# Performance work log

Measured on AMD Instinct MI355X. Metric: run time of the kernel, lower is better.

The kernel has to match this reference:

```python
import jax, jax.numpy as jnp
import numpy as np

EPS = 1e-12

def _l2norm(x):
    return x * jax.lax.rsqrt(jnp.maximum(jnp.sum(x * x, -1, keepdims=True), EPS))

def _reverse_seq(x, lens):
    # per-row reversal of the first `lens[b]` steps (tf.reverse_sequence semantics)
    T = x.shape[1]
    ar = jnp.arange(T)[None, :]
    idx = jnp.where(ar < lens[:, None], lens[:, None] - 1 - ar, ar)
    return jnp.take_along_axis(x, idx[:, :, None], axis=1)

def _lstm(x, lens, Wx, Wh, b):
    # x: [B,T,D]; outputs zeroed past lens, state frozen past lens (dynamic_rnn)
    B, T, _ = x.shape
    H = Wh.shape[0]
    xW = jnp.einsum('btd,dh->bth', x, Wx) + b  # [B,T,4H]
    def step(carry, inp):
        h, c = carry
        xw_t, t = inp
        gates = xw_t + h @ Wh
        i, f, g, o = jnp.split(gates, 4, axis=-1)
        c_new = jax.nn.sigmoid(f) * c + jax.nn.sigmoid(i) * jnp.tanh(g)
        h_new = jax.nn.sigmoid(o) * jnp.tanh(c_new)
        valid = (t < lens)[:, None]
        return (jnp.where(valid, h_new, h), jnp.where(valid, c_new, c)), jnp.where(valid, h_new, 0.0)
    z = jnp.zeros((B, H), x.dtype)
    _, outs = jax.lax.scan(step, (z, z), (xW.transpose(1, 0, 2), jnp.arange(T)))
    return outs.transpose(1, 0, 2)

def _bilstm(x, lens, Wx_f, Wh_f, b_f, Wx_b, Wh_b, b_b):
    fwd = _lstm(x, lens, Wx_f, Wh_f, b_f)
    bwd = _reverse_seq(_lstm(_reverse_seq(x, lens), lens, Wx_b, Wh_b, b_b), lens)
    return jnp.concatenate([fwd, bwd], -1)  # [B,T,2R]

def setup_inputs() -> dict:
    B, T, CTX, D, R, HA, TD = 4096, 80, 10, 300, 200, 100, 256
    V, NTOK, NTY, PL = 100000, 250, 113, 3
    ks = jax.random.split(jax.random.key(0), 16)
    f32 = jnp.float32
    return {
        'input_data': jax.random.randint(ks[0], (B, T), 0, V, jnp.int32),
        'entMentIndex': jax.random.randint(ks[1], (B, 5), 0, B * T, jnp.int32),
        'entCtxLeftIndex': jax.random.randint(ks[2], (B, CTX), 0, B * T, jnp.int32),
        'entCtxRightIndex': jax.random.randint(ks[3], (B, CTX), 0, B * T, jnp.int32),
        'entMentLent': jnp.full((B, 1), 5.0, f32),
        'ctxLeftLent': jnp.full((B, 1), float(CTX), f32),
        'ctxRightLent': jnp.full((B, 1), float(CTX), f32),
        'type_path': jax.random.randint(ks[4], (NTY, PL), 0, NTOK, jnp.int32),
        'word_embed': jax.random.normal(ks[5], (V, D), f32) * 0.1,
        'h_m': jax.random.normal(ks[6], (D, HA), f32) * 0.01,
        'h1': jax.random.normal(ks[7], (2 * R, HA), f32) * 0.01,
        'h2': jax.random.normal(ks[8], (HA, 1), f32) * 0.01,
        'Wx_f': jax.random.normal(ks[9], (D, 4 * R), f32) * 0.05,
        'Wh_f': jax.random.normal(ks[10], (R, 4 * R), f32) * 0.05,
        'b_f': jnp.zeros((4 * R,), f32),
        'Wx_b': jax.random.normal(ks[11], (D, 4 * R), f32) * 0.05,
        'Wh_b': jax.random.normal(ks[12], (R, 4 * R), f32) * 0.05,
        'b_b': jnp.zeros((4 * R,), f32),
        'dense_W': jax.random.normal(ks[13], (D + 2 * R, TD), f32) * 0.05,
        'dense_b': jnp.zeros((TD,), f32),
        'type_tok': jax.random.normal(ks[14], (NTOK, TD), f32) * 0.01,
    }

def reference(input_data, entMentIndex, entCtxLeftIndex, entCtxRightIndex,
              entMentLent, ctxLeftLent, ctxRightLent, type_path, word_embed,
              h_m, h1, h2, Wx_f, Wh_f, b_f, Wx_b, Wh_b, b_b,
              dense_W, dense_b, type_tok):
    D = word_embed.shape[1]
    # flattened sentence embeddings with zero padding row at the end
    flat = jnp.concatenate(
        [jnp.take(word_embed, input_data.reshape(-1), axis=0),
         jnp.zeros((1, D), word_embed.dtype)], 0)
    # mention feature: mean of mention word vectors
    f1 = jnp.take(flat, entMentIndex, axis=0).sum(1) / entMentLent  # [B,D]
    # context features via shared BiLSTM
    left = jnp.take(flat, entCtxLeftIndex, axis=0)
    right = jnp.take(flat, entCtxRightIndex, axis=0)
    f2 = _bilstm(left, ctxLeftLent[:, 0].astype(jnp.int32), Wx_f, Wh_f, b_f, Wx_b, Wh_b, b_b)
    f3 = _bilstm(right, ctxRightLent[:, 0].astype(jnp.int32), Wx_f, Wh_f, b_f, Wx_b, Wh_b, b_b)
    ctx = jnp.concatenate([f2, f3], 1)  # [B, 2*CTX, 2R]
    # attention pooling (non-BBN branch uses relu)
    att = jax.nn.relu(jnp.einsum('btr,rh->bth', ctx, h1) + (f1 @ h_m)[:, None, :])
    w = jax.nn.softmax((att @ h2)[:, :, 0], axis=-1)  # [B, 2*CTX]
    ctx_feat = jnp.einsum('btr,bt->br', ctx, w)
    feat = jnp.concatenate([f1, ctx_feat], 1)  # [B, D+2R]
    ent = _l2norm(jax.nn.relu(feat @ dense_W + dense_b))  # [B, TD]
    # type-path embeddings: sum token embeddings along path, l2-normalize
    type_pad = jnp.concatenate([type_tok, jnp.zeros((1, type_tok.shape[1]), type_tok.dtype)], 0)
    type_norm = _l2norm(jnp.take(type_pad, type_path, axis=0).sum(1))  # [NTY, TD]
    return ent @ type_norm.T  # [B, NTY]
```

## Files before the change

### kernel.cpp

```cpp
#include <hip/hip_runtime.h>
#include <hip/hip_bf16.h>

constexpr int B    = 4096;
constexpr int T    = 80;
constexpr int CTXN = 10;
constexpr int D    = 300;
constexpr int R    = 200;
constexpr int HA   = 100;
constexpr int TD   = 256;
constexpr int NTY  = 113;
constexpr int PL   = 3;
constexpr int NTOK = 250;
constexpr int CTX2 = 20;
constexpr int R2   = 400;
constexpr int FEAT = 700;

constexpr int XSB  = 320;
constexpr int KH   = 256;
constexpr int KW   = 576;
constexpr int NB   = 832;
constexpr int CTXS = 448;
constexpr int DREG = 224;
constexpr int F1S  = 320;
constexpr int FBS  = 704;
constexpr int FMS  = 128;
constexpr int MX   = 2 * B * CTXN;

typedef __attribute__((ext_vector_type(8))) short bf16x8;
typedef __attribute__((ext_vector_type(4))) float f32x4;

__device__ __forceinline__ ushort f2bf(float f) {
    union { float f; uint32_t u; } x{f};
    uint32_t r = x.u + 0x7fff + ((x.u >> 16) & 1);
    return (ushort)(r >> 16);
}
__device__ __forceinline__ float bf2f(ushort u) {
    union { uint32_t u; float f; } x{(uint32_t)u << 16};
    return x.f;
}
__device__ __forceinline__ float fsig(float x) {
    return __builtin_amdgcn_rcpf(1.f + __expf(-x));
}
__device__ __forceinline__ float ftanh(float x) {
    return 1.f - 2.f * __builtin_amdgcn_rcpf(__expf(2.f * x) + 1.f);
}

#define GLD_LDS(g, l) __builtin_amdgcn_global_load_lds( \
    (const __attribute__((address_space(1))) void*)(g), \
    (__attribute__((address_space(3))) void*)(l), 16, 0, 0)
#define GLD_LDS_NT(g, l) __builtin_amdgcn_global_load_lds( \
    (const __attribute__((address_space(1))) void*)(g), \
    (__attribute__((address_space(3))) void*)(l), 16, 0, 2)

constexpr int NWC = 2 * NB * KW;
__global__ void k_prepw3(const float* __restrict__ Wx_f, const float* __restrict__ Wh_f,
                         const float* __restrict__ bf_, const float* __restrict__ Wx_b,
                         const float* __restrict__ Wh_b, const float* __restrict__ bb_,
                         ushort* __restrict__ Wcat, float* __restrict__ biasb) {
    int gid = blockIdx.x * blockDim.x + threadIdx.x;
    if (gid < NWC) {
        int k = gid % KW;
        int q = gid / KW;
        int np = q % NB, dir = q / NB;
        int rb = np >> 6, g = (np >> 4) & 3, ri = np & 15;
        int r = rb * 16 + ri, col = g * 200 + r;
        float v = 0.f;
        if (r < R) {
            if (k < KH) {
                if (k < R) v = (dir ? Wh_b : Wh_f)[(size_t)k * 800 + col];
            } else {
                int kx = k - KH;
                if (kx < D) v = (dir ? Wx_b : Wx_f)[(size_t)kx * 800 + col];
            }
        }
        Wcat[gid] = f2bf(v);
    } else if (gid < NWC + 2 * NB) {
        int t = gid - NWC;
        int np = t % NB, dirb = t / NB;
        int rb = np >> 6, g = (np >> 4) & 3, ri = np & 15;
        int r = rb * 16 + ri, col = g * 200 + r;
        biasb[t] = (r < R) ? (dirb ? bb_ : bf_)[col] : 0.f;
    }
}

__global__ void k_preph1(const float* __restrict__ h1, ushort* __restrict__ h1t) {
    int gid = blockIdx.x * blockDim.x + threadIdx.x;
    if (gid >= FMS * CTXS) return;
    int k = gid % CTXS, n = gid / CTXS;
    float v = 0.f;
    if (n < HA) {
        if (k < DREG) {
            if (k < R) v = h1[(size_t)k * HA + n];
        } else {
            int r2 = k - DREG;
            if (r2 < R) v = h1[(size_t)(R + r2) * HA + n];
        }
    }
    h1t[gid] = f2bf(v);
}
__global__ void k_prephm(const float* __restrict__ h_m, ushort* __restrict__ h_mt) {
    int gid = blockIdx.x * blockDim.x + threadIdx.x;
    if (gid >= FMS * F1S) return;
    int k = gid % F1S, n = gid / F1S;
    float v = (n < HA && k < D) ? h_m[(size_t)k * HA + n] : 0.f;
    h_mt[gid] = f2bf(v);
}
__global__ void k_prepdw(const float* __restrict__ dW, ushort* __restrict__ dWt) {
    int gid = blockIdx.x * blockDim.x + threadIdx.x;
    if (gid >= TD * FBS) return;
    int k = gid % FBS, n = gid / FBS;
    float v = (k < FEAT) ? dW[(size_t)k * TD + n] : 0.f;
    dWt[gid] = f2bf(v);
}

__global__ void k_gatherb(const int* __restrict__ idxL, const int* __restrict__ idxR,
                          const int* __restrict__ input_data,
                          const float* __restrict__ we,
                          ushort* __restrict__ xb) {
    int row = blockIdx.x * 4 + (threadIdx.x >> 6);
    int lane = threadIdx.x & 63;
    if (row >= MX) return;
    int side = row / (B * CTXN);
    int bt = row % (B * CTXN);
    int idx = (side ? idxR : idxL)[bt];
    int w = (idx >= 0 && idx < B * T) ? input_data[idx] : -1;
    ushort* dst = xb + (size_t)row * XSB;
    if (lane < XSB / 8) {
        int e0 = lane * 8;
        ushort tmp[8];
        #pragma unroll
        for (int j = 0; j < 8; ++j) {
            int e = e0 + j;
            float f = (w >= 0 && e < D) ? we[(size_t)w * D + e] : 0.f;
            tmp[j] = f2bf(f);
        }
        *reinterpret_cast<bf16x8*>(dst + e0) = *reinterpret_cast<bf16x8*>(tmp);
    }
}

__global__ void k_f1(const int* __restrict__ ment_idx,
                     const float* __restrict__ ment_lent,
                     const int* __restrict__ input_data,
                     const float* __restrict__ we,
                     ushort* __restrict__ featb, ushort* __restrict__ f1b) {
    int b = blockIdx.x;
    __shared__ int wrow[5];
    if (threadIdx.x < 5) {
        int idx = ment_idx[b * 5 + threadIdx.x];
        wrow[threadIdx.x] = (idx >= 0 && idx < B * T) ? input_data[idx] : -1;
    }
    __syncthreads();
    float inv = 1.0f / ment_lent[b];
    for (int d = threadIdx.x; d < F1S; d += blockDim.x) {
        float s = 0.f;
        if (d < D) {
            #pragma unroll
            for (int j = 0; j < 5; ++j) {
                int w = wrow[j];
                if (w >= 0) s += we[(size_t)w * D + d];
            }
            s *= inv;
        }
        ushort u = f2bf(s);
        if (d < D) featb[(size_t)b * FBS + d] = u;
        f1b[(size_t)b * F1S + d] = u;
    }
}

template<int MODE>
__global__ __launch_bounds__(256) void k_mfma(
    const ushort* __restrict__ A, int lda,
    const ushort* __restrict__ Bt, int ldb,
    float* __restrict__ C, int ldc, int K,
    const float* __restrict__ aux) {
    __shared__ __align__(16) ushort As[128 * 64];
    __shared__ __align__(16) ushort Bs[64 * 64];
    int tid = threadIdx.x, wave = tid >> 6, lane = tid & 63;
    int m0 = blockIdx.y * 128, n0 = blockIdx.x * 64;
    int wr = wave >> 1, wc = wave & 1;
    f32x4 acc[4][2] = {};

    for (int k0 = 0; k0 < K; k0 += 64) {
        #pragma unroll
        for (int p = 0; p < 4; ++p) {
            int chunk = p * 4 + wave;
            int row = chunk * 8 + (lane >> 3);
            int ss = (lane & 7) ^ (row & 7);
            GLD_LDS(A + (size_t)(m0 + row) * lda + k0 + ss * 8, As + chunk * 512);
        }
        #pragma unroll
        for (int p = 0; p < 2; ++p) {
            int chunk = p * 4 + wave;
            int row = chunk * 8 + (lane >> 3);
            int ss = (lane & 7) ^ (row & 7);
            GLD_LDS(Bt + (size_t)(n0 + row) * ldb + k0 + ss * 8, Bs + chunk * 512);
        }
        __syncthreads();
        #pragma unroll
        for (int kk = 0; kk < 2; ++kk) {
            bf16x8 a[4], bf[2];
            #pragma unroll
            for (int m = 0; m < 4; ++m) {
                int r = wr * 64 + m * 16 + (lane & 15);
                int ss = (kk * 4 + (lane >> 4)) ^ (r & 7);
                a[m] = *(const bf16x8*)&As[r * 64 + ss * 8];
            }
            #pragma unroll
            for (int n = 0; n < 2; ++n) {
                int r = wc * 32 + n * 16 + (lane & 15);
                int ss = (kk * 4 + (lane >> 4)) ^ (r & 7);
                bf[n] = *(const bf16x8*)&Bs[r * 64 + ss * 8];
            }
            #pragma unroll
            for (int m = 0; m < 4; ++m)
                #pragma unroll
                for (int n = 0; n < 2; ++n)
                    acc[m][n] = __builtin_amdgcn_mfma_f32_16x16x32_bf16(a[m], bf[n], acc[m][n], 0, 0, 0);
        }
        __syncthreads();
    }
    #pragma unroll
    for (int m = 0; m < 4; ++m) {
        #pragma unroll
        for (int n = 0; n < 2; ++n) {
            int c = n0 + wc * 32 + n * 16 + (lane & 15);
            #pragma unroll
            for (int j = 0; j < 4; ++j) {
                int rr = m0 + wr * 64 + m * 16 + (lane >> 4) * 4 + j;
                float v = acc[m][n][j];
                if (MODE == 1) v = fmaxf(v + aux[c], 0.f);
                C[(size_t)rr * ldc + c] = v;
            }
        }
    }
}

__global__ __launch_bounds__(512, 1) void k_lstm(
    const ushort* __restrict__ xb,
    const ushort* __restrict__ Wcat,
    const float* __restrict__ biasb,
    const float* __restrict__ lentL, const float* __restrict__ lentR,
    ushort* __restrict__ ctxb) {
    __shared__ __align__(16) ushort hS[64 * 256];
    __shared__ __align__(16) ushort xS[64 * 320];
    __shared__ __align__(16) ushort wS[8][2][2048];
    __shared__ int lenS[64];
    __shared__ int xrowS[CTXN][64];

    const int tid = threadIdx.x, wave = tid >> 6, lane = tid & 63;
    const int bid = blockIdx.x, xcd = bid & 7;
    const int dir = xcd >> 2;
    const int idx = (xcd & 3) * 32 + (bid >> 3);
    const int side = idx >> 6, rg = idx & 63;
    const int b0 = rg * 64;
    const ushort* Wd = Wcat + (size_t)dir * NB * KW;
    const int rl = lane & 15, ch = lane >> 4;

    if (tid < 64) {
        int b = b0 + tid;
        int len = (int)((side ? lentR : lentL)[b]);
        len = min(max(len, 0), CTXN);
        lenS[tid] = len;
        for (int s = 0; s < CTXN; ++s) {
            int tt = dir ? ((s < len) ? (len - 1 - s) : s) : s;
            xrowS[s][tid] = (side * (B * CTXN) + b * CTXN + tt) * XSB;
        }
    }
    {
        uint4 zz{0, 0, 0, 0};
        for (int i = tid; i < 64 * 256 / 8; i += 512)
            reinterpret_cast<uint4*>(hS)[i] = zz;
    }

    const int nrb = (wave + 8 < 13) ? 2 : 1;
    float bias_[2][4];
    #pragma unroll
    for (int g = 0; g < 4; ++g) {
        bias_[0][g] = biasb[dir * NB + wave * 64 + g * 16 + rl];
        bias_[1][g] = (nrb > 1) ? biasb[dir * NB + (wave + 8) * 64 + g * 16 + rl] : 0.f;
    }
    float cst[2][16];
    #pragma unroll
    for (int i = 0; i < 2; ++i)
        #pragma unroll
        for (int j = 0; j < 16; ++j) cst[i][j] = 0.f;

    __syncthreads();

    #pragma unroll
    for (int i = 0; i < 5; ++i) {
        int chunk = wave * 5 + i;
        int p = chunk * 64 + lane;
        int row = p / 40, c8s = p - row * 40;
        int c8 = c8s ^ (row & 7);
        GLD_LDS_NT(xb + xrowS[0][row] + c8 * 8, xS + chunk * 512);
    }
    __syncthreads();

    float hnew[2][16];

    for (int s = 0; s < CTXN; ++s) {
        const int kstart = (s == 0) ? KH : 0;
        #pragma unroll
        for (int rbi = 0; rbi < 2; ++rbi) {
            if (rbi < nrb) {
                const int rb = rbi ? (wave + 8) : wave;
                const ushort* wb = Wd + (size_t)rb * 64 * KW;
                const int nit = (KW - kstart) >> 5;
                f32x4 acc[4][4];
                #pragma unroll
                for (int m = 0; m < 4; ++m)
                    #pragma unroll
                    for (int g = 0; g < 4; ++g) acc[m][g] = f32x4{0.f, 0.f, 0.f, 0.f};

                #pragma unroll
                for (int i = 0; i < 4; ++i) {
                    int p = i * 64 + lane;
                    int n = p >> 2, c8s = p & 3;
                    int c8 = c8s ^ ((n >> 1) & 3);
                    GLD_LDS(wb + (size_t)n * KW + kstart + c8 * 8, &wS[wave][0][0] + i * 512);
                }
                for (int t = 0; t < nit; ++t) {
                    int k0 = kstart + t * 32;
                    if (t + 1 < nit) {
                        int k1 = k0 + 32;
                        ushort* dst = &wS[wave][(t + 1) & 1][0];
                        #pragma unroll
                        for (int i = 0; i < 4; ++i) {
                            int p = i * 64 + lane;
                            int n = p >> 2, c8s = p & 3;
                            int c8 = c8s ^ ((n >> 1) & 3);
                            GLD_LDS(wb + (size_t)n * KW + k1 + c8 * 8, dst + i * 512);
                        }
                        asm volatile("s_waitcnt vmcnt(4)" ::: "memory");
                    } else {
                        asm volatile("s_waitcnt vmcnt(0)" ::: "memory");
                    }
                    const ushort* abase; int astr, kof;
                    if (k0 < KH) { abase = hS; astr = 256; kof = k0 >> 3; }
                    else         { abase = xS; astr = 320; kof = (k0 - KH) >> 3; }
                    bf16x8 af[4];
                    #pragma unroll
                    for (int m = 0; m < 4; ++m) {
                        int row = m * 16 + rl;
                        int g = (kof + ch) ^ (row & 7);
                        af[m] = *reinterpret_cast<const bf16x8*>(&abase[row * astr + g * 8]);
                    }
                    const ushort* wbuf = &wS[wave][t & 1][0];
                    bf16x8 bfr[4];
                    #pragma unroll
                    for (int g4 = 0; g4 < 4; ++g4) {
                        int col = g4 * 16 + rl;
                        int c8 = ch ^ ((rl >> 1) & 3);
                        bfr[g4] = *reinterpret_cast<const bf16x8*>(&wbuf[col * 32 + c8 * 8]);
                    }
                    #pragma unroll
                    for (int m = 0; m < 4; ++m)
                        #pragma unroll
                        for (int g4 = 0; g4 < 4; ++g4)
                            acc[m][g4] = __builtin_amdgcn_mfma_f32_16x16x32_bf16(
                                af[m], bfr[g4], acc[m][g4], 0, 0, 0);
                }
                #pragma unroll
                for (int m = 0; m < 4; ++m) {
                    #pragma unroll
                    for (int j = 0; j < 4; ++j) {
                        int row = m * 16 + ch * 4 + j;
                        float gi = acc[m][0][j] + bias_[rbi][0];
                        float gf = acc[m][1][j] + bias_[rbi][1];
                        float gg = acc[m][2][j] + bias_[rbi][2];
                        float go = acc[m][3][j] + bias_[rbi][3];
                        float si = fsig(gi), sf = fsig(gf), so = fsig(go);
                        float cn = sf * cst[rbi][m * 4 + j] + si * ftanh(gg);
                        float hn = so * ftanh(cn);
                        if (s < lenS[row]) cst[rbi][m * 4 + j] = cn;
                        hnew[rbi][m * 4 + j] = hn;
                    }
                }
            }
        }
        asm volatile("s_waitcnt lgkmcnt(0)" ::: "memory");
        __builtin_amdgcn_s_barrier();

        #pragma unroll
        for (int rbi = 0; rbi < 2; ++rbi) {
            if (rbi < nrb) {
                const int rb = wave + rbi * 8;
                const int r = rb * 16 + rl;
                #pragma unroll
                for (int m = 0; m < 4; ++m) {
                    #pragma unroll
                    for (int j = 0; j < 4; ++j) {
                        int row = m * 16 + ch * 4 + j;
                        bool live = (s < lenS[row]);
                        ushort hv = f2bf(live ? hnew[rbi][m * 4 + j] : 0.f);
                        wS[wave][1][row * 32 + rbi * 16 + rl] = hv;
                        if (live && r < R)
                            hS[row * 256 + (((r >> 3) ^ (row & 7)) << 3) + (r & 7)] = hv;
                    }
                }
            }
        }
        if (s + 1 < CTXN) {
            #pragma unroll
            for (int i = 0; i < 5; ++i) {
                int chunk = wave * 5 + i;
                int p = chunk * 64 + lane;
                int row = p / 40, c8s = p - row * 40;
                int c8 = c8s ^ (row & 7);
                GLD_LDS_NT(xb + xrowS[s + 1][row] + c8 * 8, xS + chunk * 512);
            }
        }
        asm volatile("s_waitcnt lgkmcnt(0)" ::: "memory");
        __builtin_amdgcn_s_barrier();

        for (int i = tid; i < 64 * 28; i += 512) {
            int row = i / 28, g = i - row * 28;
            int len = lenS[row];
            int tp = (s < len) ? (dir ? (len - 1 - s) : s) : s;
            bf16x8 v{};
            if (g < 26) {
                int rb2 = g >> 1;
                int w = rb2 & 7, rbi = rb2 >> 3;
                int off = (g & 1) * 8;
                v = *reinterpret_cast<const bf16x8*>(&wS[w][1][row * 32 + rbi * 16 + off]);
            }
            *reinterpret_cast<bf16x8*>(
                ctxb + ((size_t)(b0 + row) * CTX2 + side * CTXN + tp) * CTXS + dir * DREG + g * 8) = v;
        }
        asm volatile("s_waitcnt vmcnt(0) lgkmcnt(0)" ::: "memory");
        __builtin_amdgcn_s_barrier();
    }
}

__global__ __launch_bounds__(256) void k_attsc(
    const ushort* __restrict__ ctxb, const ushort* __restrict__ h1t,
    const float* __restrict__ fm, const float* __restrict__ h2,
    float* __restrict__ scores) {
    __shared__ __align__(16) ushort As[128 * 64];
    __shared__ __align__(16) ushort Bs[128 * 64];
    __shared__ float sred[128][2];
    __shared__ float h2s[128];
    int tid = threadIdx.x, wave = tid >> 6, lane = tid & 63;
    int m0 = blockIdx.x * 128;
    if (tid < 128) h2s[tid] = (tid < HA) ? h2[tid] : 0.f;
    int wr = wave >> 1, wc = wave & 1;
    f32x4 acc[4][4] = {};

    for (int k0 = 0; k0 < CTXS; k0 += 64) {
        #pragma unroll
        for (int p = 0; p < 4; ++p) {
            int chunk = p * 4 + wave;
            int row = chunk * 8 + (lane >> 3);
            int ss = (lane & 7) ^ (row & 7);
            GLD_LDS(ctxb + (size_t)(m0 + row) * CTXS + k0 + ss * 8, As + chunk * 512);
        }
        #pragma unroll
        for (int p = 0; p < 4; ++p) {
            int chunk = p * 4 + wave;
            int row = chunk * 8 + (lane >> 3);
            int ss = (lane & 7) ^ (row & 7);
            GLD_LDS(h1t + (size_t)row * CTXS + k0 + ss * 8, Bs + chunk * 512);
        }
        __syncthreads();
        #pragma unroll
        for (int kk = 0; kk < 2; ++kk) {
            bf16x8 a[4], bf[4];
            #pragma unroll
            for (int m = 0; m < 4; ++m) {
                int r = wr * 64 + m * 16 + (lane & 15);
                int ss = (kk * 4 + (lane >> 4)) ^ (r & 7);
                a[m] = *(const bf16x8*)&As[r * 64 + ss * 8];
            }
            #pragma unroll
            for (int n = 0; n < 4; ++n) {
                int r = wc * 64 + n * 16 + (lane & 15);
                int ss = (kk * 4 + (lane >> 4)) ^ (r & 7);
                bf[n] = *(const bf16x8*)&Bs[r * 64 + ss * 8];
            }
            #pragma unroll
            for (int m = 0; m < 4; ++m)
                #pragma unroll
                for (int n = 0; n < 4; ++n)
                    acc[m][n] = __builtin_amdgcn_mfma_f32_16x16x32_bf16(a[m], bf[n], acc[m][n], 0, 0, 0);
        }
        __syncthreads();
    }
    #pragma unroll
    for (int m = 0; m < 4; ++m) {
        #pragma unroll
        for (int j = 0; j < 4; ++j) {
            int rl = wr * 64 + m * 16 + (lane >> 4) * 4 + j;
            int brow = (m0 + rl) / CTX2;
            float v = 0.f;
            #pragma unroll
            for (int n = 0; n < 4; ++n) {
                int c = wc * 64 + n * 16 + (lane & 15);
                float a = acc[m][n][j] + fm[(size_t)brow * FMS + c];
                v += fmaxf(a, 0.f) * h2s[c];
            }
            #pragma unroll
            for (int o = 1; o < 16; o <<= 1) v += __shfl_xor(v, o, 64);
            if ((lane & 15) == 0) sred[rl][wc] = v;
        }
    }
    __syncthreads();
    if (tid < 128) scores[m0 + tid] = sred[tid][0] + sred[tid][1];
}

__global__ void k_att2(const float* __restrict__ scores,
                       const ushort* __restrict__ ctxb,
                       ushort* __restrict__ featb) {
    int b = blockIdx.x;
    float sc[CTX2];
    #pragma unroll
    for (int t = 0; t < CTX2; ++t) sc[t] = scores[b * CTX2 + t];
    float mx = -1e30f;
    #pragma unroll
    for (int t = 0; t < CTX2; ++t) mx = fmaxf(mx, sc[t]);
    float w[CTX2], sum = 0.f;
    #pragma unroll
    for (int t = 0; t < CTX2; ++t) { w[t] = __expf(sc[t] - mx); sum += w[t]; }
    float inv = 1.f / sum;
    for (int col = threadIdx.x; col < R2; col += 256) {
        int pos = (col < R) ? col : col + (DREG - R);
        float acc = 0.f;
        #pragma unroll
        for (int t = 0; t < CTX2; ++t)
            acc += w[t] * bf2f(ctxb[((size_t)b * CTX2 + t) * CTXS + pos]);
        featb[(size_t)b * FBS + D + col] = f2bf(acc * inv);
    }
    if (threadIdx.x < FBS - FEAT)
        featb[(size_t)b * FBS + FEAT + threadIdx.x] = 0;
}

__device__ __forceinline__ float blk_sum_256(float v, float* red) {
    #pragma unroll
    for (int o = 32; o > 0; o >>= 1) v += __shfl_down(v, o, 64);
    int lane = threadIdx.x & 63, wid = threadIdx.x >> 6;
    if (lane == 0) red[wid] = v;
    __syncthreads();
    float t = red[0] + red[1] + red[2] + red[3];
    __syncthreads();
    return t;
}

__global__ void k_l2norm(float* __restrict__ x, int ncol) {
    int row = blockIdx.x;
    float* p = x + (size_t)row * ncol;
    __shared__ float red[4];
    float ss = 0.f;
    for (int c = threadIdx.x; c < ncol; c += 256) { float v = p[c]; ss += v * v; }
    float tot = blk_sum_256(ss, red);
    float scale = 1.f / sqrtf(fmaxf(tot, 1e-12f));
    for (int c = threadIdx.x; c < ncol; c += 256) p[c] *= scale;
}

__global__ void k_typenorm(const int* __restrict__ type_path,
                           const float* __restrict__ type_tok,
                           float* __restrict__ tnorm) {
    int y = blockIdx.x;
    int c = threadIdx.x;
    __shared__ float red[4];
    float s = 0.f;
    #pragma unroll
    for (int j = 0; j < PL; ++j) {
        int tk = type_path[y * PL + j];
        if (tk >= 0 && tk < NTOK) s += type_tok[(size_t)tk * TD + c];
    }
    float tot = blk_sum_256(s * s, red);
    float scale = 1.f / sqrtf(fmaxf(tot, 1e-12f));
    tnorm[(size_t)y * TD + c] = s * scale;
}

__global__ void k_final(const float* __restrict__ ent,
                        const float* __restrict__ tnorm,
                        float* __restrict__ out) {
    int b = blockIdx.x;
    __shared__ float es[TD];
    for (int c = threadIdx.x; c < TD; c += blockDim.x) es[c] = ent[(size_t)b * TD + c];
    __syncthreads();
    for (int y = threadIdx.x; y < NTY; y += blockDim.x) {
        const float* tn = tnorm + (size_t)y * TD;
        float acc = 0.f;
        #pragma unroll 4
        for (int k = 0; k < TD; ++k) acc += es[k] * tn[k];
        out[(size_t)b * NTY + y] = acc;
    }
}

static inline char* wsalloc(char*& p, size_t bytes) {
    char* r = p;
    p += (bytes + 255) & ~(size_t)255;
    return r;
}

extern "C" void kernel_launch(void* const* d_in, const int* in_sizes, int n_in,
                              void* d_out, int out_size, void* d_ws, size_t ws_size,
                              hipStream_t stream) {
    const int*   input_data       = (const int*)d_in[0];
    const int*   entMentIndex     = (const int*)d_in[1];
    const int*   entCtxLeftIndex  = (const int*)d_in[2];
    const int*   entCtxRightIndex = (const int*)d_in[3];
    const float* entMentLent      = (const float*)d_in[4];
    const float* ctxLeftLent      = (const float*)d_in[5];
    const float* ctxRightLent     = (const float*)d_in[6];
    const int*   type_path        = (const int*)d_in[7];
    const float* word_embed       = (const float*)d_in[8];
    const float* h_m              = (const float*)d_in[9];
    const float* h1               = (const float*)d_in[10];
    const float* h2               = (const float*)d_in[11];
    const float* Wx_f             = (const float*)d_in[12];
    const float* Wh_f             = (const float*)d_in[13];
    const float* b_f              = (const float*)d_in[14];
    const float* Wx_b             = (const float*)d_in[15];
    const float* Wh_b             = (const float*)d_in[16];
    const float* b_b              = (const float*)d_in[17];
    const float* dense_W          = (const float*)d_in[18];
    const float* dense_b          = (const float*)d_in[19];
    const float* type_tok         = (const float*)d_in[20];
    float* out = (float*)d_out;

    char* p = (char*)d_ws;
    ushort* xb    = (ushort*)wsalloc(p, (size_t)MX * XSB * 2);
    ushort* ctxb  = (ushort*)wsalloc(p, (size_t)B * CTX2 * CTXS * 2);
    ushort* featb = (ushort*)wsalloc(p, (size_t)B * FBS * 2);
    ushort* f1b   = (ushort*)wsalloc(p, (size_t)B * F1S * 2);
    float*  fm    = (float*) wsalloc(p, (size_t)B * FMS * 4);
    float*  scores= (float*) wsalloc(p, (size_t)MX * 4);
    float*  ent   = (float*) wsalloc(p, (size_t)B * TD * 4);
    float*  tnorm = (float*) wsalloc(p, (size_t)NTY * TD * 4);
    ushort* Wcat  = (ushort*)wsalloc(p, (size_t)2 * NB * KW * 2);
    float*  biasb = (float*) wsalloc(p, (size_t)2 * NB * 4);
    ushort* h1t   = (ushort*)wsalloc(p, (size_t)FMS * CTXS * 2);
    ushort* h_mt  = (ushort*)wsalloc(p, (size_t)FMS * F1S * 2);
    ushort* dWt   = (ushort*)wsalloc(p, (size_t)TD * FBS * 2);

    {
        int tot = NWC + 2 * NB;
        k_prepw3<<<(tot + 255) / 256, 256, 0, stream>>>(Wx_f, Wh_f, b_f, Wx_b, Wh_b, b_b,
                                                        Wcat, biasb);
    }
    k_preph1<<<(FMS * CTXS + 255) / 256, 256, 0, stream>>>(h1, h1t);
    k_prephm<<<(FMS * F1S + 255) / 256, 256, 0, stream>>>(h_m, h_mt);
    k_prepdw<<<(TD * FBS + 255) / 256, 256, 0, stream>>>(dense_W, dWt);

    k_gatherb<<<(MX + 3) / 4, 256, 0, stream>>>(entCtxLeftIndex, entCtxRightIndex,
                                                input_data, word_embed, xb);
    k_f1<<<B, 256, 0, stream>>>(entMentIndex, entMentLent, input_data, word_embed, featb, f1b);

    k_mfma<3><<<dim3(FMS / 64, B / 128), 256, 0, stream>>>(f1b, F1S, h_mt, F1S, fm, FMS, F1S, nullptr);

    k_lstm<<<256, 512, 0, stream>>>(xb, Wcat, biasb, ctxLeftLent, ctxRightLent, ctxb);

    k_attsc<<<MX / 128, 256, 0, stream>>>(ctxb, h1t, fm, h2, scores);
    k_att2<<<B, 256, 0, stream>>>(scores, ctxb, featb);

    k_mfma<1><<<dim3(TD / 64, B / 128), 256, 0, stream>>>(featb, FBS, dWt, FBS,
                                                          ent, TD, FBS, dense_b);
    k_l2norm<<<B, 256, 0, stream>>>(ent, TD);
    k_typenorm<<<NTY, TD, 0, stream>>>(type_path, type_tok, tnorm);
    k_final<<<B, 128, 0, stream>>>(ent, tnorm, out);
}
```

Measured before the change: 555.8 us.

## Widen LSTM kernel to 16 waves, one gate row-block per wave

The recurrent LSTM kernel now launches with 1024 threads so each of 13 active waves owns a single 64-column gate block, where before 8 waves each handled up to two blocks in sequence. This removes the load imbalance in which some waves did double work per timestep. The weight streaming becomes a triple-buffered pipeline of 32-row half-tiles, with waitcnt tuned so the loads overlap the MFMA issue. In exchange, 3 of the 16 waves sit idle during the GEMM, barrier cost grows with more waves, and the per-wave register budget is tighter at 1024 threads.

```diff
diff --git a/kernel.cpp b/kernel.cpp
--- a/kernel.cpp
+++ b/kernel.cpp
@@ -235,7 +235,16 @@
     }
 }
 
-__global__ __launch_bounds__(512, 1) void k_lstm(
+#define WISSUE(KT2, HF2) { \
+    ushort* dst = &wS[wave][(2 * (KT2) + (HF2)) % 3][0]; \
+    _Pragma("unroll") for (int i = 0; i < 2; ++i) { \
+        int p = i * 64 + lane; \
+        int nl = p >> 2, c8s = p & 3; \
+        int c8 = c8s ^ ((nl >> 1) & 3); \
+        GLD_LDS(wb + (size_t)((HF2) * 32 + nl) * KW + (KT2) * 32 + c8 * 8, dst + i * 512); \
+    } }
+
+__global__ __launch_bounds__(1024, 1) void k_lstm(
     const ushort* __restrict__ xb,
     const ushort* __restrict__ Wcat,
     const float* __restrict__ biasb,
@@ -243,7 +252,7 @@
     ushort* __restrict__ ctxb) {
     __shared__ __align__(16) ushort hS[64 * 256];
     __shared__ __align__(16) ushort xS[64 * 320];
-    __shared__ __align__(16) ushort wS[8][2][2048];
+    __shared__ __align__(16) ushort wS[13][3][1024];
     __shared__ int lenS[64];
     __shared__ int xrowS[CTXN][64];
 
@@ -255,6 +264,8 @@
     const int b0 = rg * 64;
     const ushort* Wd = Wcat + (size_t)dir * NB * KW;
     const int rl = lane & 15, ch = lane >> 4;
+    const bool gw = (wave < 13);
+    const ushort* wb = gw ? (Wd + (size_t)wave * 64 * KW) : Wd;
 
     if (tid < 64) {
         int b = b0 + tid;
@@ -268,162 +279,123 @@
     }
     {
         uint4 zz{0, 0, 0, 0};
-        for (int i = tid; i < 64 * 256 / 8; i += 512)
+        for (int i = tid; i < 64 * 256 / 8; i += 1024)
             reinterpret_cast<uint4*>(hS)[i] = zz;
     }
 
-    const int nrb = (wave + 8 < 13) ? 2 : 1;
-    float bias_[2][4];
-    #pragma unroll
-    for (int g = 0; g < 4; ++g) {
-        bias_[0][g] = biasb[dir * NB + wave * 64 + g * 16 + rl];
-        bias_[1][g] = (nrb > 1) ? biasb[dir * NB + (wave + 8) * 64 + g * 16 + rl] : 0.f;
-    }
-    float cst[2][16];
-    #pragma unroll
-    for (int i = 0; i < 2; ++i)
-        #pragma unroll
-        for (int j = 0; j < 16; ++j) cst[i][j] = 0.f;
+    float bias_[4];
+    #pragma unroll
+    for (int g = 0; g < 4; ++g)
+        bias_[g] = gw ? biasb[dir * NB + wave * 64 + g * 16 + rl] : 0.f;
+    float cst[16];
+    #pragma unroll
+    for (int j = 0; j < 16; ++j) cst[j] = 0.f;
 
     __syncthreads();
 
-    #pragma unroll
-    for (int i = 0; i < 5; ++i) {
-        int chunk = wave * 5 + i;
-        int p = chunk * 64 + lane;
+    for (int c2 = wave; c2 < 40; c2 += 16) {
+        int p = c2 * 64 + lane;
         int row = p / 40, c8s = p - row * 40;
         int c8 = c8s ^ (row & 7);
-        GLD_LDS_NT(xb + xrowS[0][row] + c8 * 8, xS + chunk * 512);
+        GLD_LDS_NT(xb + xrowS[0][row] + c8 * 8, xS + c2 * 512);
     }
     __syncthreads();
 
-    float hnew[2][16];
-
     for (int s = 0; s < CTXN; ++s) {
-        const int kstart = (s == 0) ? KH : 0;
-        #pragma unroll
-        for (int rbi = 0; rbi < 2; ++rbi) {
-            if (rbi < nrb) {
-                const int rb = rbi ? (wave + 8) : wave;
-                const ushort* wb = Wd + (size_t)rb * 64 * KW;
-                const int nit = (KW - kstart) >> 5;
-                f32x4 acc[4][4];
-                #pragma unroll
-                for (int m = 0; m < 4; ++m)
-                    #pragma unroll
-                    for (int g = 0; g < 4; ++g) acc[m][g] = f32x4{0.f, 0.f, 0.f, 0.f};
-
-                #pragma unroll
-                for (int i = 0; i < 4; ++i) {
-                    int p = i * 64 + lane;
-                    int n = p >> 2, c8s = p & 3;
-                    int c8 = c8s ^ ((n >> 1) & 3);
-                    GLD_LDS(wb + (size_t)n * KW + kstart + c8 * 8, &wS[wave][0][0] + i * 512);
-                }
-                for (int t = 0; t < nit; ++t) {
-                    int k0 = kstart + t * 32;
-                    if (t + 1 < nit) {
-                        int k1 = k0 + 32;
-                        ushort* dst = &wS[wave][(t + 1) & 1][0];
-                        #pragma unroll
-                        for (int i = 0; i < 4; ++i) {
-                            int p = i * 64 + lane;
-                            int n = p >> 2, c8s = p & 3;
-                            int c8 = c8s ^ ((n >> 1) & 3);
-                            GLD_LDS(wb + (size_t)n * KW + k1 + c8 * 8, dst + i * 512);
-                        }
-                        asm volatile("s_waitcnt vmcnt(4)" ::: "memory");
-                    } else {
-                        asm volatile("s_waitcnt vmcnt(0)" ::: "memory");
-                    }
+        const int ktstart = (s == 0) ? 8 : 0;
+        f32x4 acc[4][4] = {};
+        if (gw) {
+            WISSUE(ktstart, 0);
+            WISSUE(ktstart, 1);
+            WISSUE(ktstart + 1, 0);
+            bf16x8 af[4];
+            for (int kt = ktstart; kt < 18; ++kt) {
+                {
                     const ushort* abase; int astr, kof;
-                    if (k0 < KH) { abase = hS; astr = 256; kof = k0 >> 3; }
-                    else         { abase = xS; astr = 320; kof = (k0 - KH) >> 3; }
-                    bf16x8 af[4];
+                    if (kt < 8) { abase = hS; astr = 256; kof = kt * 4; }
+                    else        { abase = xS; astr = 320; kof = (kt - 8) * 4; }
                     #pragma unroll
                     for (int m = 0; m < 4; ++m) {
                         int row = m * 16 + rl;
                         int g = (kof + ch) ^ (row & 7);
                         af[m] = *reinterpret_cast<const bf16x8*>(&abase[row * astr + g * 8]);
                     }
-                    const ushort* wbuf = &wS[wave][t & 1][0];
-                    bf16x8 bfr[4];
+                }
+                const int c8r = ch ^ ((rl >> 1) & 3);
+                if (kt < 17) { asm volatile("s_waitcnt vmcnt(4)" ::: "memory"); }
+                else         { asm volatile("s_waitcnt vmcnt(2)" ::: "memory"); }
+                {
+                    const ushort* wbuf = &wS[wave][(2 * kt) % 3][0];
+                    bf16x8 b0 = *reinterpret_cast<const bf16x8*>(&wbuf[(rl) * 32 + c8r * 8]);
+                    bf16x8 b1 = *reinterpret_cast<const bf16x8*>(&wbuf[(16 + rl) * 32 + c8r * 8]);
+                    if (kt + 1 < 18) WISSUE(kt + 1, 1);
                     #pragma unroll
-                    for (int g4 = 0; g4 < 4; ++g4) {
-                        int col = g4 * 16 + rl;
-                        int c8 = ch ^ ((rl >> 1) & 3);
-                        bfr[g4] = *reinterpret_cast<const bf16x8*>(&wbuf[col * 32 + c8 * 8]);
-                    }
-                    #pragma unroll
-                    for (int m = 0; m < 4; ++m)
-                        #pragma unroll
-                        for (int g4 = 0; g4 < 4; ++g4)
-                            acc[m][g4] = __builtin_amdgcn_mfma_f32_16x16x32_bf16(
-                                af[m], bfr[g4], acc[m][g4], 0, 0, 0);
-                }
-                #pragma unroll
-                for (int m = 0; m < 4; ++m) {
-                    #pragma unroll
-                    for (int j = 0; j < 4; ++j) {
-                        int row = m * 16 + ch * 4 + j;
-                        float gi = acc[m][0][j] + bias_[rbi][0];
-                        float gf = acc[m][1][j] + bias_[rbi][1];
-                        float gg = acc[m][2][j] + bias_[rbi][2];
-                        float go = acc[m][3][j] + bias_[rbi][3];
-                        float si = fsig(gi), sf = fsig(gf), so = fsig(go);
-                        float cn = sf * cst[rbi][m * 4 + j] + si * ftanh(gg);
-                        float hn = so * ftanh(cn);
-                        if (s < lenS[row]) cst[rbi][m * 4 + j] = cn;
-                        hnew[rbi][m * 4 + j] = hn;
+                    for (int m = 0; m < 4; ++m) {
+                        acc[m][0] = __builtin_amdgcn_mfma_f32_16x16x32_bf16(af[m], b0, acc[m][0], 0, 0, 0);
+                        acc[m][1] = __builtin_amdgcn_mfma_f32_16x16x32_bf16(af[m], b1, acc[m][1], 0, 0, 0);
                     }
                 }
+                if (kt < 17) { asm volatile("s_waitcnt vmcnt(4)" ::: "memory"); }
+                else         { asm volatile("s_waitcnt vmcnt(0)" ::: "memory"); }
+                {
+                    const ushort* wbuf = &wS[wave][(2 * kt + 1) % 3][0];
+                    bf16x8 b0 = *reinterpret_cast<const bf16x8*>(&wbuf[(rl) * 32 + c8r * 8]);
+                    bf16x8 b1 = *reinterpret_cast<const bf16x8*>(&wbuf[(16 + rl) * 32 + c8r * 8]);
+                    if (kt + 2 < 18) WISSUE(kt + 2, 0);
+                    #pragma unroll
+                    for (int m = 0; m < 4; ++m) {
+                        acc[m][2] = __builtin_amdgcn_mfma_f32_16x16x32_bf16(af[m], b0, acc[m][2], 0, 0, 0);
+                        acc[m][3] = __builtin_amdgcn_mfma_f32_16x16x32_bf16(af[m], b1, acc[m][3], 0, 0, 0);
+                    }
+                }
             }
         }
         asm volatile("s_waitcnt lgkmcnt(0)" ::: "memory");
         __builtin_amdgcn_s_barrier();
 
-        #pragma unroll
-        for (int rbi = 0; rbi < 2; ++rbi) {
-            if (rbi < nrb) {
-                const int rb = wave + rbi * 8;
-                const int r = rb * 16 + rl;
+        if (gw) {
+            const int r = wave * 16 + rl;
+            #pragma unroll
+            for (int m = 0; m < 4; ++m) {
                 #pragma unroll
-                for (int m = 0; m < 4; ++m) {
-                    #pragma unroll
-                    for (int j = 0; j < 4; ++j) {
-                        int row = m * 16 + ch * 4 + j;
-                        bool live = (s < lenS[row]);
-                        ushort hv = f2bf(live ? hnew[rbi][m * 4 + j] : 0.f);
-                        wS[wave][1][row * 32 + rbi * 16 + rl] = hv;
-                        if (live && r < R)
-                            hS[row * 256 + (((r >> 3) ^ (row & 7)) << 3) + (r & 7)] = hv;
-                    }
+                for (int j = 0; j < 4; ++j) {
+                    int row = m * 16 + ch * 4 + j;
+                    float gi = acc[m][0][j] + bias_[0];
+                    float gf = acc[m][1][j] + bias_[1];
+                    float gg = acc[m][2][j] + bias_[2];
+                    float go = acc[m][3][j] + bias_[3];
+                    float si = fsig(gi), sf = fsig(gf), so = fsig(go);
+                    float cn = sf * cst[m * 4 + j] + si * ftanh(gg);
+                    float hn = so * ftanh(cn);
+                    bool live = (s < lenS[row]);
+                    if (live) cst[m * 4 + j] = cn;
+                    ushort hv = f2bf(live ? hn : 0.f);
+                    wS[wave][0][row * 16 + rl] = hv;
+                    if (live && r < R)
+                        hS[row * 256 + (((r >> 3) ^ (row & 7)) << 3) + (r & 7)] = hv;
                 }
             }
         }
         if (s + 1 < CTXN) {
-            #pragma unroll
-            for (int i = 0; i < 5; ++i) {
-                int chunk = wave * 5 + i;
-                int p = chunk * 64 + lane;
+            for (int c2 = wave; c2 < 40; c2 += 16) {
+                int p = c2 * 64 + lane;
                 int row = p / 40, c8s = p - row * 40;
                 int c8 = c8s ^ (row & 7);
-                GLD_LDS_NT(xb + xrowS[s + 1][row] + c8 * 8, xS + chunk * 512);
+                GLD_LDS_NT(xb + xrowS[s + 1][row] + c8 * 8, xS + c2 * 512);
             }
         }
         asm volatile("s_waitcnt lgkmcnt(0)" ::: "memory");
         __builtin_amdgcn_s_barrier();
 
-        for (int i = tid; i < 64 * 28; i += 512) {
+        for (int i = tid; i < 64 * 28; i += 1024) {
             int row = i / 28, g = i - row * 28;
             int len = lenS[row];
             int tp = (s < len) ? (dir ? (len - 1 - s) : s) : s;
             bf16x8 v{};
             if (g < 26) {
                 int rb2 = g >> 1;
-                int w = rb2 & 7, rbi = rb2 >> 3;
                 int off = (g & 1) * 8;
-                v = *reinterpret_cast<const bf16x8*>(&wS[w][1][row * 32 + rbi * 16 + off]);
+                v = *reinterpret_cast<const bf16x8*>(&wS[rb2][0][row * 16 + off]);
             }
             *reinterpret_cast<bf16x8*>(
                 ctxb + ((size_t)(b0 + row) * CTX2 + side * CTXN + tp) * CTXS + dir * DREG + g * 8) = v;
@@ -651,7 +623,7 @@
 
     k_mfma<3><<<dim3(FMS / 64, B / 128), 256, 0, stream>>>(f1b, F1S, h_mt, F1S, fm, FMS, F1S, nullptr);
 
-    k_lstm<<<256, 512, 0, stream>>>(xb, Wcat, biasb, ctxLeftLent, ctxRightLent, ctxb);
+    k_lstm<<<256, 1024, 0, stream>>>(xb, Wcat, biasb, ctxLeftLent, ctxRightLent, ctxb);
 
     k_attsc<<<MX / 128, 256, 0, stream>>>(ctxb, h1t, fm, h2, scores);
     k_att2<<<B, 256, 0, stream>>>(scores, ctxb, featb);
```

Result: faster. 542.4 us (-2.4%).
